# Performance work log

Hardware: AMD Instinct MI355X
Metric: run time of the kernel (lower is better)

The kernel has to match this reference:

```python
import jax, jax.numpy as jnp
import numpy as np

N_NODES = 100000
N_EDGES = 1600000
HID = 64
N_LAYERS = 3
BN_EPS = 1e-5


def setup_inputs() -> dict:
    key = jax.random.key(0)
    ks = jax.random.split(key, 10)
    x = jax.random.normal(ks[0], (N_NODES, HID), dtype=jnp.float32)
    edge_index = jax.random.randint(ks[1], (2, N_EDGES), 0, N_NODES, dtype=jnp.int64)
    edge_atten = jax.random.uniform(ks[2], (N_EDGES, 1), dtype=jnp.float32)
    s = 1.0 / np.sqrt(HID)
    W1 = jax.random.normal(ks[3], (N_LAYERS, HID, HID), dtype=jnp.float32) * s
    b1 = jax.random.normal(ks[4], (N_LAYERS, HID), dtype=jnp.float32) * s
    gamma = jnp.ones((N_LAYERS, HID), dtype=jnp.float32)
    beta = jnp.zeros((N_LAYERS, HID), dtype=jnp.float32)
    W2 = jax.random.normal(ks[5], (N_LAYERS, HID, HID), dtype=jnp.float32) * s
    b2 = jax.random.normal(ks[6], (N_LAYERS, HID), dtype=jnp.float32) * s
    return {"x": x, "edge_index": edge_index, "edge_atten": edge_atten,
            "W1": W1, "b1": b1, "gamma": gamma, "beta": beta, "W2": W2, "b2": b2}


def reference(x, edge_index, edge_atten, W1, b1, gamma, beta, W2, b2):
    # GIN with GINConv (eps=0): out = nn(sum_{j->i} x_j * edge_atten + x_i), then ReLU
    src = edge_index[0]  # x_j gathered from source nodes
    dst = edge_index[1]  # scatter-add into target nodes
    n = x.shape[0]
    for i in range(N_LAYERS):
        msg = x[src] * edge_atten                                   # [E, H]
        agg = jax.ops.segment_sum(msg, dst, num_segments=n)         # [N, H]
        h = agg + x                                                 # (1 + eps)*x_r, eps=0
        # MLP: Linear -> BatchNorm1d (training mode, batch stats) -> ReLU -> Linear
        h = h @ W1[i] + b1[i]
        mu = jnp.mean(h, axis=0)
        var = jnp.var(h, axis=0)
        h = (h - mu) * jax.lax.rsqrt(var + BN_EPS) * gamma[i] + beta[i]
        h = jax.nn.relu(h)
        h = h @ W2[i] + b2[i]
        x = jax.nn.relu(h)  # outer self.relu after each conv
    return x
```

## Files before the change

kernel.cpp:

```cpp
#include <hip/hip_runtime.h>

#define NN 100000
#define NE 1600000
#define HID 64
#define NT (NN / 16)
#define NL 3
#define BN_EPS 1e-5f
#define BSH 7
#define BNODES 128
#define NB 782
#define GP 16
#define BIN_CHUNK 8192
#define BIN_GRID ((NE + BIN_CHUNK - 1) / BIN_CHUNK)
#define GBLK 3125
#define DCHUNK 8192
#define DGRID ((NN + DCHUNK - 1) / DCHUNK)

typedef __attribute__((ext_vector_type(8))) short short8;
typedef __attribute__((ext_vector_type(4))) float f32x4;

__device__ __forceinline__ float bf2f(unsigned short u) {
    union { unsigned int i; float f; } v; v.i = ((unsigned int)u) << 16; return v.f;
}
__device__ __forceinline__ unsigned short f2bf(float f) {
    union { float f; unsigned int i; } v; v.f = f;
    unsigned int r = v.i + 0x7FFFu + ((v.i >> 16) & 1u);
    return (unsigned short)(r >> 16);
}
__device__ __forceinline__ float lof(uint r) {
    union { uint u; float f; } v; v.u = r << 16; return v.f;
}
__device__ __forceinline__ float hif(uint r) {
    union { uint u; float f; } v; v.u = r & 0xFFFF0000u; return v.f;
}

__global__ void k_conv(const float* __restrict__ x, ushort* __restrict__ xb) {
    int i = blockIdx.x * blockDim.x + threadIdx.x;
    float4 v = ((const float4*)x)[i];
    ushort4 o;
    o.x = f2bf(v.x); o.y = f2bf(v.y); o.z = f2bf(v.z); o.w = f2bf(v.w);
    ((ushort4*)xb)[i] = o;
}

__global__ void k_wpack(const float* __restrict__ W1, const float* __restrict__ W2,
                        ushort* __restrict__ wf) {
    int s = blockIdx.x, l = threadIdx.x;
    int layer = s >> 2, kind = s & 3;
    const float* W = ((kind < 2) ? W1 : W2) + (size_t)layer * HID * HID;
    ushort* o = wf + (size_t)s * 4096;
    for (int kh = 0; kh < 2; ++kh)
        for (int t = 0; t < 4; ++t)
            for (int j = 0; j < 8; ++j) {
                int k = kh * 32 + (l >> 4) * 8 + j;
                int n = t * 16 + (l & 15);
                float f = W[k * HID + n];
                ushort hi = f2bf(f);
                o[((kh * 4 + t) * 64 + l) * 8 + j] =
                    (kind & 1) ? f2bf(f - bf2f(hi)) : hi;
            }
}

__global__ __launch_bounds__(1024) void k_histB(const int* __restrict__ dst,
                                                int* __restrict__ ghist) {
    __shared__ int lh[NB];
    int tid = threadIdx.x;
    for (int i = tid; i < NB; i += 1024) lh[i] = 0;
    __syncthreads();
    int base = blockIdx.x * BIN_CHUNK;
    int end = min(base + BIN_CHUNK, NE);
    for (int e = base + tid * 4; e + 3 < end; e += 4096) {
        int4 d = *(const int4*)(dst + e);
        atomicAdd(&lh[d.x >> BSH], 1);
        atomicAdd(&lh[d.y >> BSH], 1);
        atomicAdd(&lh[d.z >> BSH], 1);
        atomicAdd(&lh[d.w >> BSH], 1);
    }
    __syncthreads();
    for (int i = tid; i < NB; i += 1024)
        if (lh[i]) atomicAdd(&ghist[i * GP], lh[i]);
}

__global__ void k_scanB(const int* __restrict__ ghist, int* __restrict__ boffB,
                        int* __restrict__ gcur) {
    __shared__ int t[1024];
    int tid = threadIdx.x;
    int v = (tid < NB) ? ghist[tid * GP] : 0;
    t[tid] = v;
    __syncthreads();
    for (int d = 1; d < 1024; d <<= 1) {
        int u = (tid >= d) ? t[tid - d] : 0;
        __syncthreads();
        t[tid] += u;
        __syncthreads();
    }
    if (tid < NB) { int ex = t[tid] - v; boffB[tid] = ex; gcur[tid * GP] = ex; }
    if (tid == 0) boffB[NB] = NE;
}

__global__ __launch_bounds__(1024) void k_binB(const int* __restrict__ ei,
                                               const float* __restrict__ att,
                                               int* __restrict__ gcur,
                                               int2* __restrict__ evb) {
    __shared__ int lh[NB];
    int tid = threadIdx.x;
    for (int i = tid; i < NB; i += 1024) lh[i] = 0;
    __syncthreads();
    int base = blockIdx.x * BIN_CHUNK;
    int end = min(base + BIN_CHUNK, NE);
    for (int e = base + tid * 4; e + 3 < end; e += 4096) {
        int4 d = *(const int4*)(ei + NE + e);
        atomicAdd(&lh[d.x >> BSH], 1);
        atomicAdd(&lh[d.y >> BSH], 1);
        atomicAdd(&lh[d.z >> BSH], 1);
        atomicAdd(&lh[d.w >> BSH], 1);
    }
    __syncthreads();
    for (int i = tid; i < NB; i += 1024) {
        int c = lh[i];
        lh[i] = c ? atomicAdd(&gcur[i * GP], c) : 0;
    }
    __syncthreads();
    for (int e = base + tid * 4; e + 3 < end; e += 4096) {
        int4 s = *(const int4*)(ei + e);
        int4 d = *(const int4*)(ei + NE + e);
        float4 a = *(const float4*)(att + e);
        int p0 = atomicAdd(&lh[d.x >> BSH], 1);
        int p1 = atomicAdd(&lh[d.y >> BSH], 1);
        int p2 = atomicAdd(&lh[d.z >> BSH], 1);
        int p3 = atomicAdd(&lh[d.w >> BSH], 1);
        evb[p0] = make_int2(s.x | ((d.x & (BNODES - 1)) << 17), __float_as_int(a.x));
        evb[p1] = make_int2(s.y | ((d.y & (BNODES - 1)) << 17), __float_as_int(a.y));
        evb[p2] = make_int2(s.z | ((d.z & (BNODES - 1)) << 17), __float_as_int(a.z));
        evb[p3] = make_int2(s.w | ((d.w & (BNODES - 1)) << 17), __float_as_int(a.w));
    }
}

__global__ __launch_bounds__(256) void k_scatter2(const int2* __restrict__ evb,
                                                  const int* __restrict__ boffB,
                                                  int* __restrict__ offs,
                                                  uint* __restrict__ evc) {
    __shared__ int h[BNODES];
    __shared__ int cur[BNODES];
    int tid = threadIdx.x;
    int b = blockIdx.x;
    int node0 = b << BSH;
    int nvalid = min(BNODES, NN - node0);
    int e0 = boffB[b], e1 = boffB[b + 1];
    if (tid < BNODES) h[tid] = 0;
    __syncthreads();
    for (int e = e0 + tid * 2; e < e1; e += 512) {
        int2 r0 = evb[e];
        int v1 = (e + 1 < e1);
        int2 r1 = evb[v1 ? e + 1 : e];
        atomicAdd(&h[r0.x >> 17], 1);
        if (v1) atomicAdd(&h[r1.x >> 17], 1);
    }
    __syncthreads();
    int v = (tid < BNODES) ? h[tid] : 0;
    for (int d = 1; d < BNODES; d <<= 1) {
        int u = (tid >= d && tid < BNODES) ? h[tid - d] : 0;
        __syncthreads();
        if (tid < BNODES) h[tid] += u;
        __syncthreads();
    }
    if (tid < BNODES) {
        int start = e0 + h[tid] - v;
        cur[tid] = start;
        if (tid < nvalid) offs[node0 + tid] = start;
    }
    if (b == NB - 1 && tid == 0) offs[NN] = NE;
    __syncthreads();
    for (int e = e0 + tid * 2; e < e1; e += 512) {
        int2 r0 = evb[e];
        int v1 = (e + 1 < e1);
        int2 r1 = evb[v1 ? e + 1 : e];
        int p0 = atomicAdd(&cur[r0.x >> 17], 1);
        int p1 = v1 ? atomicAdd(&cur[r1.x >> 17], 1) : 0;
        uint a0 = (uint)(__int_as_float(r0.y) * 32767.0f + 0.5f);
        evc[p0] = ((uint)r0.x & 0x1FFFFu) | (a0 << 17);
        if (v1) {
            uint a1 = (uint)(__int_as_float(r1.y) * 32767.0f + 0.5f);
            evc[p1] = ((uint)r1.x & 0x1FFFFu) | (a1 << 17);
        }
    }
}

__global__ __launch_bounds__(1024) void k_dhist(const int* __restrict__ offs,
                                                int* __restrict__ dh) {
    __shared__ int lh[256];
    int tid = threadIdx.x;
    if (tid < 256) lh[tid] = 0;
    __syncthreads();
    int lo = blockIdx.x * DCHUNK, hi = min(lo + DCHUNK, NN);
    for (int i = lo + tid; i < hi; i += 1024)
        atomicAdd(&lh[min(offs[i + 1] - offs[i], 255)], 1);
    __syncthreads();
    if (tid < 256 && lh[tid]) atomicAdd(&dh[tid * GP], lh[tid]);
}

__global__ void k_dscan(const int* __restrict__ dh, int* __restrict__ dcur) {
    __shared__ int t[256];
    int tid = threadIdx.x;
    int v = dh[tid * GP];
    t[tid] = v;
    __syncthreads();
    for (int d = 1; d < 256; d <<= 1) {
        int u = (tid >= d) ? t[tid - d] : 0;
        __syncthreads();
        t[tid] += u;
        __syncthreads();
    }
    dcur[tid * GP] = t[tid] - v;
}

__global__ __launch_bounds__(1024) void k_dplace(const int* __restrict__ offs,
                                                 int* __restrict__ dcur,
                                                 int* __restrict__ perm) {
    __shared__ int lh[256];
    __shared__ int lbase[256];
    int tid = threadIdx.x;
    if (tid < 256) lh[tid] = 0;
    __syncthreads();
    int lo = blockIdx.x * DCHUNK, hi = min(lo + DCHUNK, NN);
    int mybin[8], myrk[8];
#pragma unroll 8
    for (int u = 0; u < 8; ++u) {
        int i = lo + u * 1024 + tid;
        if (i < hi) {
            int b = min(offs[i + 1] - offs[i], 255);
            mybin[u] = b;
            myrk[u] = atomicAdd(&lh[b], 1);
        } else mybin[u] = -1;
    }
    __syncthreads();
    if (tid < 256) {
        int c = lh[tid];
        lbase[tid] = c ? atomicAdd(&dcur[tid * GP], c) : 0;
    }
    __syncthreads();
#pragma unroll 8
    for (int u = 0; u < 8; ++u) {
        int i = lo + u * 1024 + tid;
        if (mybin[u] >= 0) perm[lbase[mybin[u]] + myrk[u]] = i;
    }
}

__global__ __launch_bounds__(256, 4) void k_gather(const ushort* __restrict__ xb,
                                                   const int* __restrict__ offs,
                                                   const uint* __restrict__ evc,
                                                   const int* __restrict__ perm,
                                                   ushort* __restrict__ agg) {
    int tid = threadIdx.x;
    int wid = blockIdx.x * 4 + (tid >> 6);
    int lane = tid & 63;
    int g = lane >> 3, k = lane & 7;
    const uint4* xq4 = (const uint4*)xb;
    uint4* aq4 = (uint4*)agg;
    int node = perm[wid * 8 + g];
    int e0 = offs[node], e1 = offs[node + 1];
    int deg = e1 - e0;
    uint4 s4 = xq4[(size_t)node * 8 + k];
    float ax0 = lof(s4.x), ay0 = hif(s4.x);
    float ax1 = lof(s4.y), ay1 = hif(s4.y);
    float ax2 = lof(s4.z), ay2 = hif(s4.z);
    float ax3 = lof(s4.w), ay3 = hif(s4.w);
    int maxd = deg;
    maxd = max(maxd, __shfl_xor(maxd, 8, 64));
    maxd = max(maxd, __shfl_xor(maxd, 16, 64));
    maxd = max(maxd, __shfl_xor(maxd, 32, 64));
    for (int base = 0; base < maxd; base += 8) {
        uint ew = evc[min(e0 + base + k, NE - 1)];
#pragma unroll 8
        for (int j = 0; j < 8; ++j) {
            uint w = (uint)__builtin_amdgcn_ds_bpermute((g * 8 + j) << 2, (int)ew);
            float a = (base + j < deg) ? (float)(w >> 17) * (1.0f / 32767.0f) : 0.f;
            uint4 r = xq4[(size_t)(w & 0x1FFFF) * 8 + k];
            ax0 += lof(r.x) * a; ay0 += hif(r.x) * a;
            ax1 += lof(r.y) * a; ay1 += hif(r.y) * a;
            ax2 += lof(r.z) * a; ay2 += hif(r.z) * a;
            ax3 += lof(r.w) * a; ay3 += hif(r.w) * a;
        }
    }
    uint4 o;
    o.x = ((uint)f2bf(ax0)) | (((uint)f2bf(ay0)) << 16);
    o.y = ((uint)f2bf(ax1)) | (((uint)f2bf(ay1)) << 16);
    o.z = ((uint)f2bf(ax2)) | (((uint)f2bf(ay2)) << 16);
    o.w = ((uint)f2bf(ax3)) | (((uint)f2bf(ay3)) << 16);
    aq4[(size_t)node * 8 + k] = o;
}

__global__ __launch_bounds__(256, 2) void k_mlp1(const ushort* __restrict__ aggc,
                                                 const ushort* __restrict__ wfb,
                                                 const float* __restrict__ b1,
                                                 ushort* __restrict__ h,
                                                 float* __restrict__ stats) {
    __shared__ float red1[4][64], red2[4][64];
    int tid = threadIdx.x, wv = tid >> 6, l = tid & 63;
    int lg = l >> 4, lc = l & 15;
    short8 bhi[2][4], blo[2][4];
#pragma unroll
    for (int kh = 0; kh < 2; ++kh)
#pragma unroll
        for (int t = 0; t < 4; ++t) {
            bhi[kh][t] = *(const short8*)(wfb + ((kh * 4 + t) * 64 + l) * 8);
            blo[kh][t] = *(const short8*)(wfb + 4096 + ((kh * 4 + t) * 64 + l) * 8);
        }
    f32x4 bias4[4];
#pragma unroll
    for (int t = 0; t < 4; ++t) {
        float4 bv = *(const float4*)(b1 + t * 16 + lg * 4);
        bias4[t] = (f32x4){bv.x, bv.y, bv.z, bv.w};
    }
    float s1[16], s2[16];
#pragma unroll
    for (int i = 0; i < 16; ++i) { s1[i] = 0.f; s2[i] = 0.f; }
    int gw = blockIdx.x * 4 + wv, nw = gridDim.x * 4;
    for (int tile = gw; tile < NT; tile += nw) {
        int node = tile * 16 + lc;
        const ushort* ap = aggc + (size_t)node * HID + lg * 8;
        short8 a0 = *(const short8*)ap;
        short8 a1 = *(const short8*)(ap + 32);
        f32x4 acc[4];
#pragma unroll
        for (int t = 0; t < 4; ++t) {
            acc[t] = bias4[t];
            acc[t] = __builtin_amdgcn_mfma_f32_16x16x32_bf16(bhi[0][t], a0, acc[t], 0, 0, 0);
            acc[t] = __builtin_amdgcn_mfma_f32_16x16x32_bf16(bhi[1][t], a1, acc[t], 0, 0, 0);
            acc[t] = __builtin_amdgcn_mfma_f32_16x16x32_bf16(blo[0][t], a0, acc[t], 0, 0, 0);
            acc[t] = __builtin_amdgcn_mfma_f32_16x16x32_bf16(blo[1][t], a1, acc[t], 0, 0, 0);
        }
#pragma unroll
        for (int t = 0; t < 4; ++t) {
            ushort4 o;
            float d0 = acc[t][0], d1 = acc[t][1], d2 = acc[t][2], d3 = acc[t][3];
            s1[t * 4 + 0] += d0; s2[t * 4 + 0] += d0 * d0;
            s1[t * 4 + 1] += d1; s2[t * 4 + 1] += d1 * d1;
            s1[t * 4 + 2] += d2; s2[t * 4 + 2] += d2 * d2;
            s1[t * 4 + 3] += d3; s2[t * 4 + 3] += d3 * d3;
            o.x = f2bf(d0); o.y = f2bf(d1); o.z = f2bf(d2); o.w = f2bf(d3);
            *(ushort4*)(h + (size_t)node * HID + t * 16 + lg * 4) = o;
        }
    }
#pragma unroll
    for (int i = 0; i < 16; ++i) {
        s1[i] += __shfl_xor(s1[i], 1, 64); s1[i] += __shfl_xor(s1[i], 2, 64);
        s1[i] += __shfl_xor(s1[i], 4, 64); s1[i] += __shfl_xor(s1[i], 8, 64);
        s2[i] += __shfl_xor(s2[i], 1, 64); s2[i] += __shfl_xor(s2[i], 2, 64);
        s2[i] += __shfl_xor(s2[i], 4, 64); s2[i] += __shfl_xor(s2[i], 8, 64);
    }
    if (lc == 0) {
#pragma unroll
        for (int t = 0; t < 4; ++t)
#pragma unroll
            for (int r = 0; r < 4; ++r) {
                red1[wv][t * 16 + lg * 4 + r] = s1[t * 4 + r];
                red2[wv][t * 16 + lg * 4 + r] = s2[t * 4 + r];
            }
    }
    __syncthreads();
    if (tid < 64)
        atomicAdd(&stats[tid], red1[0][tid] + red1[1][tid] + red1[2][tid] + red1[3][tid]);
    else if (tid < 128) {
        int c = tid - 64;
        atomicAdd(&stats[HID + c], red2[0][c] + red2[1][c] + red2[2][c] + red2[3][c]);
    }
}

__global__ __launch_bounds__(256, 2) void k_mlp2(const ushort* __restrict__ wfb,
                                                 const float* __restrict__ b2,
                                                 const float* __restrict__ gamma,
                                                 const float* __restrict__ beta,
                                                 const float* __restrict__ stats,
                                                 const ushort* __restrict__ h,
                                                 ushort* __restrict__ xb_out,
                                                 float* __restrict__ f_out,
                                                 int write_f32) {
    int tid = threadIdx.x, wv = tid >> 6, l = tid & 63;
    int lg = l >> 4, lc = l & 15;
    short8 bhi[2][4], blo[2][4];
#pragma unroll
    for (int kh = 0; kh < 2; ++kh)
#pragma unroll
        for (int t = 0; t < 4; ++t) {
            bhi[kh][t] = *(const short8*)(wfb + 8192 + ((kh * 4 + t) * 64 + l) * 8);
            blo[kh][t] = *(const short8*)(wfb + 12288 + ((kh * 4 + t) * 64 + l) * 8);
        }
    f32x4 bias4[4];
#pragma unroll
    for (int t = 0; t < 4; ++t) {
        float4 bv = *(const float4*)(b2 + t * 16 + lg * 4);
        bias4[t] = (f32x4){bv.x, bv.y, bv.z, bv.w};
    }
    float aCk[2][8], bCk[2][8];
#pragma unroll
    for (int kh = 0; kh < 2; ++kh)
#pragma unroll
        for (int j = 0; j < 8; ++j) {
            int k = kh * 32 + lg * 8 + j;
            float mu = stats[k] * (1.0f / NN);
            float var = fmaxf(stats[HID + k] * (1.0f / NN) - mu * mu, 0.f);
            float aC = gamma[k] * rsqrtf(var + BN_EPS);
            aCk[kh][j] = aC;
            bCk[kh][j] = beta[k] - mu * aC;
        }
    int gw = blockIdx.x * 4 + wv, nw = gridDim.x * 4;
    for (int tile = gw; tile < NT; tile += nw) {
        int node = tile * 16 + lc;
        const ushort* hp = h + (size_t)node * HID + lg * 8;
        short8 a0r = *(const short8*)hp;
        short8 a1r = *(const short8*)(hp + 32);
        short8 a0, a1;
#pragma unroll
        for (int j = 0; j < 8; ++j) {
            float v0 = fmaxf(aCk[0][j] * bf2f((ushort)a0r[j]) + bCk[0][j], 0.f);
            float v1 = fmaxf(aCk[1][j] * bf2f((ushort)a1r[j]) + bCk[1][j], 0.f);
            a0[j] = (short)f2bf(v0);
            a1[j] = (short)f2bf(v1);
        }
        f32x4 acc[4];
#pragma unroll
        for (int t = 0; t < 4; ++t) {
            acc[t] = bias4[t];
            acc[t] = __builtin_amdgcn_mfma_f32_16x16x32_bf16(bhi[0][t], a0, acc[t], 0, 0, 0);
            acc[t] = __builtin_amdgcn_mfma_f32_16x16x32_bf16(bhi[1][t], a1, acc[t], 0, 0, 0);
            acc[t] = __builtin_amdgcn_mfma_f32_16x16x32_bf16(blo[0][t], a0, acc[t], 0, 0, 0);
            acc[t] = __builtin_amdgcn_mfma_f32_16x16x32_bf16(blo[1][t], a1, acc[t], 0, 0, 0);
        }
        if (write_f32) {
#pragma unroll
            for (int t = 0; t < 4; ++t) {
                float4 o4;
                o4.x = fmaxf(acc[t][0], 0.f); o4.y = fmaxf(acc[t][1], 0.f);
                o4.z = fmaxf(acc[t][2], 0.f); o4.w = fmaxf(acc[t][3], 0.f);
                *(float4*)(f_out + (size_t)node * HID + t * 16 + lg * 4) = o4;
            }
        } else {
#pragma unroll
            for (int t = 0; t < 4; ++t) {
                ushort4 o;
                o.x = f2bf(fmaxf(acc[t][0], 0.f)); o.y = f2bf(fmaxf(acc[t][1], 0.f));
                o.z = f2bf(fmaxf(acc[t][2], 0.f)); o.w = f2bf(fmaxf(acc[t][3], 0.f));
                *(ushort4*)(xb_out + (size_t)node * HID + t * 16 + lg * 4) = o;
            }
        }
    }
}

extern "C" void kernel_launch(void* const* d_in, const int* in_sizes, int n_in,
                              void* d_out, int out_size, void* d_ws, size_t ws_size,
                              hipStream_t stream) {
    const float* x_in  = (const float*)d_in[0];
    const int*   ei    = (const int*)d_in[1];
    const float* att   = (const float*)d_in[2];
    const float* W1    = (const float*)d_in[3];
    const float* b1    = (const float*)d_in[4];
    const float* gamma = (const float*)d_in[5];
    const float* beta  = (const float*)d_in[6];
    const float* W2    = (const float*)d_in[7];
    const float* b2    = (const float*)d_in[8];
    float* out = (float*)d_out;

    char* ws = (char*)d_ws;
    size_t off = 0;
    auto alloc = [&](size_t bytes) -> void* {
        void* p = ws + off;
        off += (bytes + 255) & ~(size_t)255;
        return p;
    };
    ushort* xb    = (ushort*)alloc((size_t)NN * HID * 2);
    ushort* aggb  = (ushort*)alloc((size_t)NN * HID * 2);
    ushort* hb    = (ushort*)alloc((size_t)NN * HID * 2);
    ushort* wf    = (ushort*)alloc((size_t)12 * 4096 * 2);
    int*    ghist = (int*)alloc((size_t)NB * GP * 4);
    int*    boffB = (int*)alloc((size_t)(NB + 1) * 4);
    int*    gcur  = (int*)alloc((size_t)NB * GP * 4);
    int*    offs  = (int*)alloc((size_t)(NN + 1) * 4);
    int2*   evb   = (int2*)alloc((size_t)NE * 8);
    uint*   evc   = (uint*)alloc((size_t)NE * 4);
    int*    dh    = (int*)alloc((size_t)256 * GP * 4);
    int*    dcur  = (int*)alloc((size_t)256 * GP * 4);
    int*    perm  = (int*)alloc((size_t)NN * 4);
    float*  stats = (float*)alloc(NL * 128 * 4);

    hipMemsetAsync(ghist, 0, (size_t)NB * GP * 4, stream);
    hipMemsetAsync(dh, 0, (size_t)256 * GP * 4, stream);
    hipMemsetAsync(stats, 0, NL * 128 * 4, stream);

    k_conv<<<(NN * HID / 4 + 255) / 256, 256, 0, stream>>>(x_in, xb);
    k_wpack<<<12, 64, 0, stream>>>(W1, W2, wf);
    k_histB<<<BIN_GRID, 1024, 0, stream>>>(ei + NE, ghist);
    k_scanB<<<1, 1024, 0, stream>>>(ghist, boffB, gcur);
    k_binB<<<BIN_GRID, 1024, 0, stream>>>(ei, att, gcur, evb);
    k_scatter2<<<NB, 256, 0, stream>>>(evb, boffB, offs, evc);
    k_dhist<<<DGRID, 1024, 0, stream>>>(offs, dh);
    k_dscan<<<1, 256, 0, stream>>>(dh, dcur);
    k_dplace<<<DGRID, 1024, 0, stream>>>(offs, dcur, perm);

    for (int l = 0; l < NL; ++l) {
        const ushort* wfb = wf + (size_t)l * 4 * 4096;
        k_gather<<<GBLK, 256, 0, stream>>>(xb, offs, evc, perm, aggb);
        k_mlp1<<<1024, 256, 0, stream>>>(aggb, wfb, b1 + l * HID, hb, stats + l * 128);
        k_mlp2<<<1024, 256, 0, stream>>>(wfb, b2 + l * HID,
                                         gamma + l * HID, beta + l * HID,
                                         stats + l * 128, hb,
                                         xb, out, (l == NL - 1) ? 1 : 0);
    }
}
```

Measured before the change: 332.6 us.

## Reuse per-block bin counts, fold degree histogram into scatter, pack gather math

The histogram kernel now stores each block's per-bin counts, so the binning kernel reads them instead of re-reading destinations and recounting with shared atomics. The separate degree-histogram kernel is removed; the scatter kernel adds each node's degree to the global histogram directly with global atomics. The gather kernel is moved to float2 accumulators, which may allow packed FMA, and its occupancy hint goes from 4 to 6. This saves a launch and a pass over the edge destinations, at the cost of an extra scratch buffer, more global atomic contention on the degree bins, and tighter register pressure in the gather.

Result: slower. 502.2 us (+51.0%).

```diff
diff --git a/kernel.cpp b/kernel.cpp
--- a/kernel.cpp
+++ b/kernel.cpp
@@ -32,6 +32,9 @@
 }
 __device__ __forceinline__ float hif(uint r) {
     union { uint u; float f; } v; v.u = r & 0xFFFF0000u; return v.f;
+}
+__device__ __forceinline__ float2 cvt2(uint u) {
+    return make_float2(lof(u), hif(u));
 }
 
 __global__ void k_conv(const float* __restrict__ x, ushort* __restrict__ xb) {
@@ -61,7 +64,8 @@
 }
 
 __global__ __launch_bounds__(1024) void k_histB(const int* __restrict__ dst,
-                                                int* __restrict__ ghist) {
+                                                int* __restrict__ ghist,
+                                                int* __restrict__ pcnt) {
     __shared__ int lh[NB];
     int tid = threadIdx.x;
     for (int i = tid; i < NB; i += 1024) lh[i] = 0;
@@ -76,8 +80,12 @@
         atomicAdd(&lh[d.w >> BSH], 1);
     }
     __syncthreads();
-    for (int i = tid; i < NB; i += 1024)
-        if (lh[i]) atomicAdd(&ghist[i * GP], lh[i]);
+    int* prow = pcnt + (size_t)blockIdx.x * NB;
+    for (int i = tid; i < NB; i += 1024) {
+        int c = lh[i];
+        prow[i] = c;
+        if (c) atomicAdd(&ghist[i * GP], c);
+    }
 }
 
 __global__ void k_scanB(const int* __restrict__ ghist, int* __restrict__ boffB,
@@ -99,27 +107,19 @@
 
 __global__ __launch_bounds__(1024) void k_binB(const int* __restrict__ ei,
                                                const float* __restrict__ att,
+                                               const int* __restrict__ pcnt,
                                                int* __restrict__ gcur,
                                                int2* __restrict__ evb) {
     __shared__ int lh[NB];
     int tid = threadIdx.x;
-    for (int i = tid; i < NB; i += 1024) lh[i] = 0;
+    const int* prow = pcnt + (size_t)blockIdx.x * NB;
+    for (int i = tid; i < NB; i += 1024) {
+        int c = prow[i];
+        lh[i] = c ? atomicAdd(&gcur[i * GP], c) : 0;
+    }
     __syncthreads();
     int base = blockIdx.x * BIN_CHUNK;
     int end = min(base + BIN_CHUNK, NE);
-    for (int e = base + tid * 4; e + 3 < end; e += 4096) {
-        int4 d = *(const int4*)(ei + NE + e);
-        atomicAdd(&lh[d.x >> BSH], 1);
-        atomicAdd(&lh[d.y >> BSH], 1);
-        atomicAdd(&lh[d.z >> BSH], 1);
-        atomicAdd(&lh[d.w >> BSH], 1);
-    }
-    __syncthreads();
-    for (int i = tid; i < NB; i += 1024) {
-        int c = lh[i];
-        lh[i] = c ? atomicAdd(&gcur[i * GP], c) : 0;
-    }
-    __syncthreads();
     for (int e = base + tid * 4; e + 3 < end; e += 4096) {
         int4 s = *(const int4*)(ei + e);
         int4 d = *(const int4*)(ei + NE + e);
@@ -138,7 +138,8 @@
 __global__ __launch_bounds__(256) void k_scatter2(const int2* __restrict__ evb,
                                                   const int* __restrict__ boffB,
                                                   int* __restrict__ offs,
-                                                  uint* __restrict__ evc) {
+                                                  uint* __restrict__ evc,
+                                                  int* __restrict__ dh) {
     __shared__ int h[BNODES];
     __shared__ int cur[BNODES];
     int tid = threadIdx.x;
@@ -157,6 +158,7 @@
     }
     __syncthreads();
     int v = (tid < BNODES) ? h[tid] : 0;
+    if (tid < nvalid) atomicAdd(&dh[min(v, 255) * GP], 1);
     for (int d = 1; d < BNODES; d <<= 1) {
         int u = (tid >= d && tid < BNODES) ? h[tid - d] : 0;
         __syncthreads();
@@ -185,19 +187,6 @@
     }
 }
 
-__global__ __launch_bounds__(1024) void k_dhist(const int* __restrict__ offs,
-                                                int* __restrict__ dh) {
-    __shared__ int lh[256];
-    int tid = threadIdx.x;
-    if (tid < 256) lh[tid] = 0;
-    __syncthreads();
-    int lo = blockIdx.x * DCHUNK, hi = min(lo + DCHUNK, NN);
-    for (int i = lo + tid; i < hi; i += 1024)
-        atomicAdd(&lh[min(offs[i + 1] - offs[i], 255)], 1);
-    __syncthreads();
-    if (tid < 256 && lh[tid]) atomicAdd(&dh[tid * GP], lh[tid]);
-}
-
 __global__ void k_dscan(const int* __restrict__ dh, int* __restrict__ dcur) {
     __shared__ int t[256];
     int tid = threadIdx.x;
@@ -245,7 +234,7 @@
     }
 }
 
-__global__ __launch_bounds__(256, 4) void k_gather(const ushort* __restrict__ xb,
+__global__ __launch_bounds__(256, 6) void k_gather(const ushort* __restrict__ xb,
                                                    const int* __restrict__ offs,
                                                    const uint* __restrict__ evc,
                                                    const int* __restrict__ perm,
@@ -260,10 +249,7 @@
     int e0 = offs[node], e1 = offs[node + 1];
     int deg = e1 - e0;
     uint4 s4 = xq4[(size_t)node * 8 + k];
-    float ax0 = lof(s4.x), ay0 = hif(s4.x);
-    float ax1 = lof(s4.y), ay1 = hif(s4.y);
-    float ax2 = lof(s4.z), ay2 = hif(s4.z);
-    float ax3 = lof(s4.w), ay3 = hif(s4.w);
+    float2 A0 = cvt2(s4.x), A1 = cvt2(s4.y), A2 = cvt2(s4.z), A3 = cvt2(s4.w);
     int maxd = deg;
     maxd = max(maxd, __shfl_xor(maxd, 8, 64));
     maxd = max(maxd, __shfl_xor(maxd, 16, 64));
@@ -274,18 +260,19 @@
         for (int j = 0; j < 8; ++j) {
             uint w = (uint)__builtin_amdgcn_ds_bpermute((g * 8 + j) << 2, (int)ew);
             float a = (base + j < deg) ? (float)(w >> 17) * (1.0f / 32767.0f) : 0.f;
+            float2 av = make_float2(a, a);
             uint4 r = xq4[(size_t)(w & 0x1FFFF) * 8 + k];
-            ax0 += lof(r.x) * a; ay0 += hif(r.x) * a;
-            ax1 += lof(r.y) * a; ay1 += hif(r.y) * a;
-            ax2 += lof(r.z) * a; ay2 += hif(r.z) * a;
-            ax3 += lof(r.w) * a; ay3 += hif(r.w) * a;
+            A0 += cvt2(r.x) * av;
+            A1 += cvt2(r.y) * av;
+            A2 += cvt2(r.z) * av;
+            A3 += cvt2(r.w) * av;
         }
     }
     uint4 o;
-    o.x = ((uint)f2bf(ax0)) | (((uint)f2bf(ay0)) << 16);
-    o.y = ((uint)f2bf(ax1)) | (((uint)f2bf(ay1)) << 16);
-    o.z = ((uint)f2bf(ax2)) | (((uint)f2bf(ay2)) << 16);
-    o.w = ((uint)f2bf(ax3)) | (((uint)f2bf(ay3)) << 16);
+    o.x = ((uint)f2bf(A0.x)) | (((uint)f2bf(A0.y)) << 16);
+    o.y = ((uint)f2bf(A1.x)) | (((uint)f2bf(A1.y)) << 16);
+    o.z = ((uint)f2bf(A2.x)) | (((uint)f2bf(A2.y)) << 16);
+    o.w = ((uint)f2bf(A3.x)) | (((uint)f2bf(A3.y)) << 16);
     aq4[(size_t)node * 8 + k] = o;
 }
 
@@ -474,6 +461,7 @@
     int*    ghist = (int*)alloc((size_t)NB * GP * 4);
     int*    boffB = (int*)alloc((size_t)(NB + 1) * 4);
     int*    gcur  = (int*)alloc((size_t)NB * GP * 4);
+    int*    pcnt  = (int*)alloc((size_t)BIN_GRID * NB * 4);
     int*    offs  = (int*)alloc((size_t)(NN + 1) * 4);
     int2*   evb   = (int2*)alloc((size_t)NE * 8);
     uint*   evc   = (uint*)alloc((size_t)NE * 4);
@@ -488,11 +476,10 @@
 
     k_conv<<<(NN * HID / 4 + 255) / 256, 256, 0, stream>>>(x_in, xb);
     k_wpack<<<12, 64, 0, stream>>>(W1, W2, wf);
-    k_histB<<<BIN_GRID, 1024, 0, stream>>>(ei + NE, ghist);
+    k_histB<<<BIN_GRID, 1024, 0, stream>>>(ei + NE, ghist, pcnt);
     k_scanB<<<1, 1024, 0, stream>>>(ghist, boffB, gcur);
-    k_binB<<<BIN_GRID, 1024, 0, stream>>>(ei, att, gcur, evb);
-    k_scatter2<<<NB, 256, 0, stream>>>(evb, boffB, offs, evc);
-    k_dhist<<<DGRID, 1024, 0, stream>>>(offs, dh);
+    k_binB<<<BIN_GRID, 1024, 0, stream>>>(ei, att, pcnt, gcur, evb);
+    k_scatter2<<<NB, 256, 0, stream>>>(evb, boffB, offs, evc, dh);
     k_dscan<<<1, 256, 0, stream>>>(dh, dcur);
     k_dplace<<<DGRID, 1024, 0, stream>>>(offs, dcur, perm);
 
```
